# Kernel tuning notes

Measured on AMD Instinct MI355X. Metric: run time of the kernel, lower is better.

The kernel has to match this reference:

```python
import jax, jax.numpy as jnp
import numpy as np

B, D, OUT, K = 2048, 256, 256, 16


def setup_inputs() -> dict:
    key = jax.random.key(0)
    k1, k2, k3, k4 = jax.random.split(key, 4)
    x = jax.random.normal(k1, (B, D), dtype=jnp.float32)
    values = jax.random.uniform(k2, (OUT, D, K), dtype=jnp.float32, minval=-0.05, maxval=0.05)
    skip_w = jax.random.normal(k3, (OUT, D), dtype=jnp.float32) * (1.0 / np.sqrt(D).astype(np.float32))
    skip_b = jax.random.normal(k4, (OUT,), dtype=jnp.float32) * 0.01
    return {"x": x, "values": values, "skip_w": skip_w, "skip_b": skip_b}


def reference(x, values, skip_w, skip_b):
    # x: (B, D); values: (OUT, D, K); skip_w: (OUT, D); skip_b: (OUT,)
    num_knots = values.shape[-1]
    grid = jnp.linspace(-1.0, 1.0, num_knots)  # (K,)
    xc = jnp.clip(x, -1.0, 1.0)
    # torch.bucketize(x, grid) with right=False == searchsorted side='left'
    right = jnp.searchsorted(grid, xc, side='left')
    left = jnp.clip(right - 1, 0, num_knots - 2)  # (B, D)
    right = left + 1
    g0 = grid[left]
    g1 = grid[right]
    w = (xc - g0) / (g1 - g0 + 1e-12)  # (B, D)
    # Gather spline values per (sample, input-dim) knot bucket.
    vt = jnp.transpose(values, (1, 2, 0))  # (D, K, OUT)
    dim_idx = jnp.arange(xc.shape[1])[None, :]  # (1, D)
    v_left = vt[dim_idx, left]    # (B, D, OUT)
    v_right = vt[dim_idx, right]  # (B, D, OUT)
    # Linear interpolation + sum over input dims.
    y = jnp.sum((1.0 - w)[..., None] * v_left + w[..., None] * v_right, axis=1)  # (B, OUT)
    # Skip connection on the clamped input (torch reassigns x = clamp(x) first).
    return y + xc @ skip_w.T + skip_b
```

## Files before the change

### kernel.cpp

```cpp
#include <hip/hip_runtime.h>
#include <hip/hip_bf16.h>


namespace {
constexpr int Bsz  = 2048;
constexpr int Din  = 256;
constexpr int Dout = 256;
constexpr int Kn   = 16;
constexpr int KKNOT = Din * Kn;
constexpr int Ksp   = KKNOT + Din;
constexpr float INV_H = 7.5f;
constexpr float Hgrid = 2.0f / 15.0f;

constexpr int BM = 128, BN = 128, BK = 64;
constexpr int TOTSTEP = Ksp / BK;
constexpr int NSPLIT  = 17;
constexpr int MT = Bsz / BM;
constexpr int NT = Dout / BN;
}

typedef __attribute__((ext_vector_type(8))) short shortx8;
typedef __attribute__((ext_vector_type(4))) float floatx4;
typedef __attribute__((address_space(3))) unsigned int lds_u32;
typedef __attribute__((address_space(1))) const unsigned int gbl_u32;

__device__ __forceinline__ unsigned int f2bf(float f) {
  __hip_bfloat16 h = __float2bfloat16(f);
  return (unsigned int)*reinterpret_cast<unsigned short*>(&h);
}

__global__ __launch_bounds__(256) void build_wt(
    const float* __restrict__ values, const float* __restrict__ skip_w,
    unsigned short* __restrict__ Wt) {
  const int c = blockIdx.x * 256 + threadIdx.x;
  const float* src;
  unsigned short* dst;
  if (c < KKNOT * Dout / 8) {
    const int o = c >> 9, i = c & 511;
    src = values + (size_t)c * 8;
    dst = Wt + (size_t)o * Ksp + i * 8;
  } else {
    const int c2 = c - KKNOT * Dout / 8;
    const int o = c2 >> 5, i = c2 & 31;
    src = skip_w + (size_t)c2 * 8;
    dst = Wt + (size_t)o * Ksp + KKNOT + i * 8;
  }
  const float4 v0 = *(const float4*)src;
  const float4 v1 = *(const float4*)(src + 4);
  const unsigned int u0 = f2bf(v0.x) | (f2bf(v0.y) << 16);
  const unsigned int u1 = f2bf(v0.z) | (f2bf(v0.w) << 16);
  const unsigned int u2 = f2bf(v1.x) | (f2bf(v1.y) << 16);
  const unsigned int u3 = f2bf(v1.z) | (f2bf(v1.w) << 16);
  *(uint4*)dst = make_uint4(u0, u1, u2, u3);
}

__global__ __launch_bounds__(256) void kan_gemm(
    const float* __restrict__ x, const unsigned short* __restrict__ Wt,
    float* __restrict__ part) {
  __shared__ __align__(16) unsigned short As[BM][BK];
  __shared__ __align__(16) unsigned short Bs[BN][BK];

  const int tid = threadIdx.x;
  const int ks  = blockIdx.x % NSPLIT;
  const int nt  = (blockIdx.x / NSPLIT) % NT;
  const int mt  = blockIdx.x / (NSPLIT * NT);
  const int m0 = mt * BM, n0 = nt * BN;
  const int g0 = ks * (TOTSTEP / NSPLIT), g1 = g0 + TOTSTEP / NSPLIT;

  const int row  = tid & 127;
  const int half = tid >> 7;
  const int b    = m0 + row;

  const int wave = tid >> 6, lane = tid & 63;
  const int wm = (wave & 1) * 64, wn = (wave >> 1) * 64;
  const int lrow = lane & 15, lq = lane >> 4;

  floatx4 acc[4][4] = {};

  for (int g = g0; g < g1; ++g) {
    __syncthreads();

    #pragma unroll
    for (int p = 0; p < 4; ++p) {
      const int c = tid + p * 256;
      const int n = c >> 3, kcs = c & 7;
      const int kc = kcs ^ (n & 7);
      const unsigned short* gsrc = Wt + (size_t)(n0 + n) * Ksp + g * 64 + kc * 8;
      unsigned int* l = (unsigned int*)(&Bs[0][0]) + c * 4;
      __builtin_amdgcn_global_load_lds((gbl_u32*)gsrc, (lds_u32*)l, 16, 0, 0);
    }

    unsigned int u[16];
    if (g < KKNOT / BK) {
      const float2 tt = *(const float2*)(x + (size_t)b * Din + g * 4 + 2 * half);
      const float t0 = (fminf(1.f, fmaxf(-1.f, tt.x)) + 1.f) * INV_H;
      const float t1 = (fminf(1.f, fmaxf(-1.f, tt.y)) + 1.f) * INV_H;
      #pragma unroll
      for (int i = 0; i < 8; ++i) {
        const float a0 = fmaxf(0.f, 1.f - fabsf(t0 - (float)(2 * i)));
        const float a1 = fmaxf(0.f, 1.f - fabsf(t0 - (float)(2 * i + 1)));
        u[i] = f2bf(a0) | (f2bf(a1) << 16);
        const float b0 = fmaxf(0.f, 1.f - fabsf(t1 - (float)(2 * i)));
        const float b1 = fmaxf(0.f, 1.f - fabsf(t1 - (float)(2 * i + 1)));
        u[8 + i] = f2bf(b0) | (f2bf(b1) << 16);
      }
    } else {
      const int off = (g - KKNOT / BK) * 64 + half * 32;
      const float4* xq = (const float4*)(x + (size_t)b * Din + off);
      #pragma unroll
      for (int q = 0; q < 8; ++q) {
        const float4 v = xq[q];
        u[2 * q]     = f2bf(fminf(1.f, fmaxf(-1.f, v.x))) | (f2bf(fminf(1.f, fmaxf(-1.f, v.y))) << 16);
        u[2 * q + 1] = f2bf(fminf(1.f, fmaxf(-1.f, v.z))) | (f2bf(fminf(1.f, fmaxf(-1.f, v.w))) << 16);
      }
    }
    #pragma unroll
    for (int j = 0; j < 4; ++j) {
      const int slot = (half * 4 + j) ^ (row & 7);
      *(uint4*)((char*)(&As[0][0]) + row * 128 + slot * 16) =
          make_uint4(u[4 * j], u[4 * j + 1], u[4 * j + 2], u[4 * j + 3]);
    }

    __syncthreads();

    shortx8 af[4][2], bfr[4][2];
    #pragma unroll
    for (int i = 0; i < 4; ++i) {
      const int r = wm + 16 * i + lrow;
      #pragma unroll
      for (int kk = 0; kk < 2; ++kk) {
        const int slot = (kk * 4 + lq) ^ (r & 7);
        af[i][kk] = *(const shortx8*)((const char*)(&As[0][0]) + r * 128 + slot * 16);
      }
    }
    #pragma unroll
    for (int j = 0; j < 4; ++j) {
      const int r = wn + 16 * j + lrow;
      #pragma unroll
      for (int kk = 0; kk < 2; ++kk) {
        const int slot = (kk * 4 + lq) ^ (r & 7);
        bfr[j][kk] = *(const shortx8*)((const char*)(&Bs[0][0]) + r * 128 + slot * 16);
      }
    }
    #pragma unroll
    for (int kk = 0; kk < 2; ++kk)
      #pragma unroll
      for (int i = 0; i < 4; ++i)
        #pragma unroll
        for (int j = 0; j < 4; ++j)
          acc[i][j] = __builtin_amdgcn_mfma_f32_16x16x32_bf16(af[i][kk], bfr[j][kk], acc[i][j], 0, 0, 0);
  }

  float* P = part + (size_t)ks * Bsz * Dout;
  #pragma unroll
  for (int i = 0; i < 4; ++i) {
    const int grow = m0 + wm + 16 * i + lq * 4;
    #pragma unroll
    for (int j = 0; j < 4; ++j) {
      const int gcol = n0 + wn + 16 * j + lrow;
      #pragma unroll
      for (int r = 0; r < 4; ++r)
        P[(size_t)(grow + r) * Dout + gcol] = acc[i][j][r];
    }
  }
}

__global__ __launch_bounds__(256) void kan_reduce(
    const float* __restrict__ part, const float* __restrict__ skip_b,
    float* __restrict__ out) {
  const int i = blockIdx.x * 256 + threadIdx.x;
  const int base = i * 4;
  const int o = base & (Dout - 1);
  float4 a = *(const float4*)(skip_b + o);
  #pragma unroll
  for (int s = 0; s < NSPLIT; ++s) {
    const float4 p = *(const float4*)(part + (size_t)s * Bsz * Dout + base);
    a.x += p.x; a.y += p.y; a.z += p.z; a.w += p.w;
  }
  *(float4*)(out + base) = a;
}

__device__ __forceinline__ void knot_interp(float xraw, float& xv, float& w, int& l) {
  xv = fminf(1.0f, fmaxf(-1.0f, xraw));
  float t = (xv + 1.0f) * INV_H;
  l = (int)ceilf(t) - 1;
  l = l < 0 ? 0 : (l > Kn - 2 ? Kn - 2 : l);
  float g0 = -1.0f + Hgrid * (float)l;
  w = (xv - g0) * INV_H;
}

__global__ __launch_bounds__(256) void prep_transpose(
    const float* __restrict__ values, const float* __restrict__ skip_w,
    float* __restrict__ vt, float* __restrict__ swt) {
  int idx = blockIdx.x * blockDim.x + threadIdx.x;
  if (idx < Din * Kn * Dout) {
    int k = idx & (Kn - 1);
    int d = (idx >> 4) & (Din - 1);
    int o = idx >> 12;
    vt[(d * Kn + k) * Dout + o] = values[idx];
  }
  if (idx < Dout * Din) {
    int d = idx & (Din - 1);
    int o = idx >> 8;
    swt[d * Dout + o] = skip_w[idx];
  }
}

__global__ __launch_bounds__(256) void kan_main(
    const float* __restrict__ x, const float* __restrict__ vt,
    const float* __restrict__ swt, const float* __restrict__ skip_b,
    float* __restrict__ out) {
  __shared__ float s_w[4][Din];
  __shared__ float s_x[4][Din];
  __shared__ int   s_l[4][Din];
  const int tid = threadIdx.x;
  const int b0  = blockIdx.x * 4;
  for (int i = tid; i < 4 * Din; i += 256) {
    int bb = i >> 8;
    int d  = i & (Din - 1);
    float xv, w; int l;
    knot_interp(x[(b0 + bb) * Din + d], xv, w, l);
    s_w[bb][d] = w; s_x[bb][d] = xv; s_l[bb][d] = l;
  }
  __syncthreads();
  const int g = tid >> 6, lane = tid & 63;
  const int o = lane << 2, b = b0 + g;
  float4 acc = make_float4(0.f, 0.f, 0.f, 0.f);
  for (int d = 0; d < Din; ++d) {
    const float w = s_w[g][d], xv = s_x[g][d];
    const int l = s_l[g][d];
    const float* base = vt + (d * Kn + l) * Dout + o;
    const float4 vl = *(const float4*)(base);
    const float4 vr = *(const float4*)(base + Dout);
    const float4 sw = *(const float4*)(swt + d * Dout + o);
    acc.x = fmaf(xv, sw.x, fmaf(w, vr.x - vl.x, acc.x + vl.x));
    acc.y = fmaf(xv, sw.y, fmaf(w, vr.y - vl.y, acc.y + vl.y));
    acc.z = fmaf(xv, sw.z, fmaf(w, vr.z - vl.z, acc.z + vl.z));
    acc.w = fmaf(xv, sw.w, fmaf(w, vr.w - vl.w, acc.w + vl.w));
  }
  const float4 bias = *(const float4*)(skip_b + o);
  acc.x += bias.x; acc.y += bias.y; acc.z += bias.z; acc.w += bias.w;
  *(float4*)(out + (size_t)b * Dout + o) = acc;
}

extern "C" void kernel_launch(void* const* d_in, const int* in_sizes, int n_in,
                              void* d_out, int out_size, void* d_ws, size_t ws_size,
                              hipStream_t stream) {
  (void)in_sizes; (void)n_in; (void)out_size;
  const float* x      = (const float*)d_in[0];
  const float* values = (const float*)d_in[1];
  const float* skip_w = (const float*)d_in[2];
  const float* skip_b = (const float*)d_in[3];
  float* out = (float*)d_out;

  const size_t wt_bytes   = (size_t)Dout * Ksp * sizeof(unsigned short);
  const size_t part_bytes = (size_t)NSPLIT * Bsz * Dout * sizeof(float);
  const size_t need_gemm  = wt_bytes + part_bytes;
  const size_t need_fb    = (size_t)(Din * Kn * Dout + Din * Dout) * sizeof(float);

  if (ws_size >= need_gemm) {
    unsigned short* Wt = (unsigned short*)d_ws;
    float* part = (float*)((char*)d_ws + wt_bytes);
    build_wt<<<(KKNOT * Dout / 8 + Din * Dout / 8 + 255) / 256, 256, 0, stream>>>(values, skip_w, Wt);
    kan_gemm<<<MT * NT * NSPLIT, 256, 0, stream>>>(x, Wt, part);
    kan_reduce<<<Bsz * Dout / 4 / 256, 256, 0, stream>>>(part, skip_b, out);
  } else if (ws_size >= need_fb) {
    float* vt  = (float*)d_ws;
    float* swt = vt + Din * Kn * Dout;
    prep_transpose<<<(Din * Kn * Dout + 255) / 256, 256, 0, stream>>>(values, skip_w, vt, swt);
    kan_main<<<Bsz / 4, 256, 0, stream>>>(x, vt, swt, skip_b, out);
  }
}
```

Measured before the change: 85.14 us.

## Prepack weights into MFMA fragment layout and drop LDS from GEMM

The weight prep kernel now writes bf16 weights directly in the per-lane MFMA B-fragment order, so each wave loads its B operand straight from global memory into registers without staging in LDS. The hat-basis A fragments are generated per lane in registers. The GEMM moves to independent 64x64 per-wave tiles with register double-buffering and no __syncthreads. The split-K factor drops from 17 to 8, which shrinks the partial buffer the reduce kernel has to read. The trade-off is that the block-level operand reuse LDS provided is gone, so each wave does more global and L2 loads and recomputes its basis values.

Measured after the change: 102.2 us. +20.0%, slower.

```diff
diff --git a/kernel.cpp b/kernel.cpp
--- a/kernel.cpp
+++ b/kernel.cpp
@@ -9,155 +9,144 @@
 constexpr int Kn   = 16;
 constexpr int KKNOT = Din * Kn;
 constexpr int Ksp   = KKNOT + Din;
+constexpr int KB    = Ksp / 32;
 constexpr float INV_H = 7.5f;
 constexpr float Hgrid = 2.0f / 15.0f;
 
-constexpr int BM = 128, BN = 128, BK = 64;
-constexpr int TOTSTEP = Ksp / BK;
-constexpr int NSPLIT  = 17;
-constexpr int MT = Bsz / BM;
-constexpr int NT = Dout / BN;
+constexpr int NSPLIT = 8;
+constexpr int SPS    = KB / NSPLIT;
 }
 
 typedef __attribute__((ext_vector_type(8))) short shortx8;
 typedef __attribute__((ext_vector_type(4))) float floatx4;
-typedef __attribute__((address_space(3))) unsigned int lds_u32;
-typedef __attribute__((address_space(1))) const unsigned int gbl_u32;
 
 __device__ __forceinline__ unsigned int f2bf(float f) {
   __hip_bfloat16 h = __float2bfloat16(f);
   return (unsigned int)*reinterpret_cast<unsigned short*>(&h);
 }
-
-__global__ __launch_bounds__(256) void build_wt(
+__device__ __forceinline__ float clamp1(float v) {
+  return fminf(1.f, fmaxf(-1.f, v));
+}
+
+union FragCvt { uint4 u; shortx8 s; };
+
+__global__ __launch_bounds__(256) void kan_prep(
     const float* __restrict__ values, const float* __restrict__ skip_w,
-    unsigned short* __restrict__ Wt) {
-  const int c = blockIdx.x * 256 + threadIdx.x;
-  const float* src;
-  unsigned short* dst;
-  if (c < KKNOT * Dout / 8) {
-    const int o = c >> 9, i = c & 511;
-    src = values + (size_t)c * 8;
-    dst = Wt + (size_t)o * Ksp + i * 8;
-  } else {
-    const int c2 = c - KKNOT * Dout / 8;
-    const int o = c2 >> 5, i = c2 & 31;
-    src = skip_w + (size_t)c2 * 8;
-    dst = Wt + (size_t)o * Ksp + KKNOT + i * 8;
-  }
+    unsigned short* __restrict__ Wf) {
+  const int tid = blockIdx.x * 256 + threadIdx.x;
+  const int q  = tid & 3;
+  const int n  = (tid >> 2) & 15;
+  const int og = (tid >> 6) & 15;
+  const int kb = tid >> 10;
+  const int o  = og * 16 + n;
+  const int k0 = kb * 32 + q * 8;
+  const float* src = (kb < KKNOT / 32)
+      ? values + (size_t)o * KKNOT + k0
+      : skip_w + (size_t)o * Din + (k0 - KKNOT);
   const float4 v0 = *(const float4*)src;
   const float4 v1 = *(const float4*)(src + 4);
-  const unsigned int u0 = f2bf(v0.x) | (f2bf(v0.y) << 16);
-  const unsigned int u1 = f2bf(v0.z) | (f2bf(v0.w) << 16);
-  const unsigned int u2 = f2bf(v1.x) | (f2bf(v1.y) << 16);
-  const unsigned int u3 = f2bf(v1.z) | (f2bf(v1.w) << 16);
-  *(uint4*)dst = make_uint4(u0, u1, u2, u3);
+  const size_t chunk = (size_t)kb * 1024 + og * 64 + q * 16 + n;
+  *(uint4*)(Wf + chunk * 8) = make_uint4(
+      f2bf(v0.x) | (f2bf(v0.y) << 16), f2bf(v0.z) | (f2bf(v0.w) << 16),
+      f2bf(v1.x) | (f2bf(v1.y) << 16), f2bf(v1.z) | (f2bf(v1.w) << 16));
 }
 
 __global__ __launch_bounds__(256) void kan_gemm(
-    const float* __restrict__ x, const unsigned short* __restrict__ Wt,
+    const float* __restrict__ x, const unsigned short* __restrict__ Wf,
     float* __restrict__ part) {
-  __shared__ __align__(16) unsigned short As[BM][BK];
-  __shared__ __align__(16) unsigned short Bs[BN][BK];
-
-  const int tid = threadIdx.x;
-  const int ks  = blockIdx.x % NSPLIT;
-  const int nt  = (blockIdx.x / NSPLIT) % NT;
-  const int mt  = blockIdx.x / (NSPLIT * NT);
-  const int m0 = mt * BM, n0 = nt * BN;
-  const int g0 = ks * (TOTSTEP / NSPLIT), g1 = g0 + TOTSTEP / NSPLIT;
-
-  const int row  = tid & 127;
-  const int half = tid >> 7;
-  const int b    = m0 + row;
-
+  const int tid  = threadIdx.x;
   const int wave = tid >> 6, lane = tid & 63;
-  const int wm = (wave & 1) * 64, wn = (wave >> 1) * 64;
+  const int gw   = blockIdx.x * 4 + wave;
+  const int ks   = gw & 7;
+  const int ni   = (gw >> 3) & 3;
+  const int mi   = gw >> 5;
+  const int m0   = mi * 64;
+  const int og0  = ni * 4;
+  const int kb0  = ks * SPS, kb1 = kb0 + SPS;
+
   const int lrow = lane & 15, lq = lane >> 4;
+  const int dsel = lq >> 1;
+  const float hbase = (float)((lq & 1) * 8);
+
+  const uint4* B = (const uint4*)Wf;
 
   floatx4 acc[4][4] = {};
-
-  for (int g = g0; g < g1; ++g) {
-    __syncthreads();
-
+  uint4 bb[2][4];
+  float xs[2][4];
+
+  #pragma unroll
+  for (int j = 0; j < 4; ++j) bb[0][j] = B[(size_t)kb0 * 1024 + (og0 + j) * 64 + lane];
+  if (kb0 < KKNOT / 32) {
     #pragma unroll
-    for (int p = 0; p < 4; ++p) {
-      const int c = tid + p * 256;
-      const int n = c >> 3, kcs = c & 7;
-      const int kc = kcs ^ (n & 7);
-      const unsigned short* gsrc = Wt + (size_t)(n0 + n) * Ksp + g * 64 + kc * 8;
-      unsigned int* l = (unsigned int*)(&Bs[0][0]) + c * 4;
-      __builtin_amdgcn_global_load_lds((gbl_u32*)gsrc, (lds_u32*)l, 16, 0, 0);
-    }
-
-    unsigned int u[16];
-    if (g < KKNOT / BK) {
-      const float2 tt = *(const float2*)(x + (size_t)b * Din + g * 4 + 2 * half);
-      const float t0 = (fminf(1.f, fmaxf(-1.f, tt.x)) + 1.f) * INV_H;
-      const float t1 = (fminf(1.f, fmaxf(-1.f, tt.y)) + 1.f) * INV_H;
-      #pragma unroll
-      for (int i = 0; i < 8; ++i) {
-        const float a0 = fmaxf(0.f, 1.f - fabsf(t0 - (float)(2 * i)));
-        const float a1 = fmaxf(0.f, 1.f - fabsf(t0 - (float)(2 * i + 1)));
-        u[i] = f2bf(a0) | (f2bf(a1) << 16);
-        const float b0 = fmaxf(0.f, 1.f - fabsf(t1 - (float)(2 * i)));
-        const float b1 = fmaxf(0.f, 1.f - fabsf(t1 - (float)(2 * i + 1)));
-        u[8 + i] = f2bf(b0) | (f2bf(b1) << 16);
+    for (int i = 0; i < 4; ++i)
+      xs[0][i] = x[(size_t)(m0 + 16 * i + lrow) * Din + kb0 * 2 + dsel];
+  }
+
+  for (int s = 0; s < SPS; ++s) {
+    const int kb = kb0 + s;
+    const int cur = s & 1, nxt = cur ^ 1;
+
+    if (s + 1 < SPS) {
+      const int kn = kb + 1;
+      #pragma unroll
+      for (int j = 0; j < 4; ++j) bb[nxt][j] = B[(size_t)kn * 1024 + (og0 + j) * 64 + lane];
+      if (kn < KKNOT / 32) {
+        #pragma unroll
+        for (int i = 0; i < 4; ++i)
+          xs[nxt][i] = x[(size_t)(m0 + 16 * i + lrow) * Din + kn * 2 + dsel];
+      }
+    }
+
+    shortx8 af[4];
+    if (kb < KKNOT / 32) {
+      #pragma unroll
+      for (int i = 0; i < 4; ++i) {
+        const float t = (clamp1(xs[cur][i]) + 1.f) * INV_H;
+        FragCvt c;
+        unsigned int uu[4];
+        #pragma unroll
+        for (int p = 0; p < 4; ++p) {
+          const float e0 = fmaxf(0.f, 1.f - fabsf(t - (hbase + (float)(2 * p))));
+          const float e1 = fmaxf(0.f, 1.f - fabsf(t - (hbase + (float)(2 * p + 1))));
+          uu[p] = f2bf(e0) | (f2bf(e1) << 16);
+        }
+        c.u = make_uint4(uu[0], uu[1], uu[2], uu[3]);
+        af[i] = c.s;
       }
     } else {
-      const int off = (g - KKNOT / BK) * 64 + half * 32;
-      const float4* xq = (const float4*)(x + (size_t)b * Din + off);
-      #pragma unroll
-      for (int q = 0; q < 8; ++q) {
-        const float4 v = xq[q];
-        u[2 * q]     = f2bf(fminf(1.f, fmaxf(-1.f, v.x))) | (f2bf(fminf(1.f, fmaxf(-1.f, v.y))) << 16);
-        u[2 * q + 1] = f2bf(fminf(1.f, fmaxf(-1.f, v.z))) | (f2bf(fminf(1.f, fmaxf(-1.f, v.w))) << 16);
+      const int xoff = (kb - KKNOT / 32) * 32 + lq * 8;
+      #pragma unroll
+      for (int i = 0; i < 4; ++i) {
+        const float* xp = x + (size_t)(m0 + 16 * i + lrow) * Din + xoff;
+        const float4 v0 = *(const float4*)xp;
+        const float4 v1 = *(const float4*)(xp + 4);
+        FragCvt c;
+        c.u = make_uint4(
+            f2bf(clamp1(v0.x)) | (f2bf(clamp1(v0.y)) << 16),
+            f2bf(clamp1(v0.z)) | (f2bf(clamp1(v0.w)) << 16),
+            f2bf(clamp1(v1.x)) | (f2bf(clamp1(v1.y)) << 16),
+            f2bf(clamp1(v1.z)) | (f2bf(clamp1(v1.w)) << 16));
+        af[i] = c.s;
       }
     }
+
     #pragma unroll
     for (int j = 0; j < 4; ++j) {
-      const int slot = (half * 4 + j) ^ (row & 7);
-      *(uint4*)((char*)(&As[0][0]) + row * 128 + slot * 16) =
-          make_uint4(u[4 * j], u[4 * j + 1], u[4 * j + 2], u[4 * j + 3]);
-    }
-
-    __syncthreads();
-
-    shortx8 af[4][2], bfr[4][2];
-    #pragma unroll
-    for (int i = 0; i < 4; ++i) {
-      const int r = wm + 16 * i + lrow;
-      #pragma unroll
-      for (int kk = 0; kk < 2; ++kk) {
-        const int slot = (kk * 4 + lq) ^ (r & 7);
-        af[i][kk] = *(const shortx8*)((const char*)(&As[0][0]) + r * 128 + slot * 16);
-      }
-    }
-    #pragma unroll
-    for (int j = 0; j < 4; ++j) {
-      const int r = wn + 16 * j + lrow;
-      #pragma unroll
-      for (int kk = 0; kk < 2; ++kk) {
-        const int slot = (kk * 4 + lq) ^ (r & 7);
-        bfr[j][kk] = *(const shortx8*)((const char*)(&Bs[0][0]) + r * 128 + slot * 16);
-      }
-    }
-    #pragma unroll
-    for (int kk = 0; kk < 2; ++kk)
+      FragCvt bc; bc.u = bb[cur][j];
+      const shortx8 bf = bc.s;
       #pragma unroll
       for (int i = 0; i < 4; ++i)
-        #pragma unroll
-        for (int j = 0; j < 4; ++j)
-          acc[i][j] = __builtin_amdgcn_mfma_f32_16x16x32_bf16(af[i][kk], bfr[j][kk], acc[i][j], 0, 0, 0);
+        acc[i][j] = __builtin_amdgcn_mfma_f32_16x16x32_bf16(af[i], bf, acc[i][j], 0, 0, 0);
+    }
   }
 
   float* P = part + (size_t)ks * Bsz * Dout;
   #pragma unroll
   for (int i = 0; i < 4; ++i) {
-    const int grow = m0 + wm + 16 * i + lq * 4;
+    const int grow = m0 + 16 * i + lq * 4;
     #pragma unroll
     for (int j = 0; j < 4; ++j) {
-      const int gcol = n0 + wn + 16 * j + lrow;
+      const int gcol = og0 * 16 + 16 * j + lrow;
       #pragma unroll
       for (int r = 0; r < 4; ++r)
         P[(size_t)(grow + r) * Dout + gcol] = acc[i][j][r];
@@ -253,16 +242,16 @@
   const float* skip_b = (const float*)d_in[3];
   float* out = (float*)d_out;
 
-  const size_t wt_bytes   = (size_t)Dout * Ksp * sizeof(unsigned short);
+  const size_t wf_bytes   = (size_t)Dout * Ksp * sizeof(unsigned short);
   const size_t part_bytes = (size_t)NSPLIT * Bsz * Dout * sizeof(float);
-  const size_t need_gemm  = wt_bytes + part_bytes;
+  const size_t need_gemm  = wf_bytes + part_bytes;
   const size_t need_fb    = (size_t)(Din * Kn * Dout + Din * Dout) * sizeof(float);
 
   if (ws_size >= need_gemm) {
-    unsigned short* Wt = (unsigned short*)d_ws;
-    float* part = (float*)((char*)d_ws + wt_bytes);
-    build_wt<<<(KKNOT * Dout / 8 + Din * Dout / 8 + 255) / 256, 256, 0, stream>>>(values, skip_w, Wt);
-    kan_gemm<<<MT * NT * NSPLIT, 256, 0, stream>>>(x, Wt, part);
+    unsigned short* Wf = (unsigned short*)d_ws;
+    float* part = (float*)((char*)d_ws + wf_bytes);
+    kan_prep<<<(KB * 1024) / 256, 256, 0, stream>>>(values, skip_w, Wf);
+    kan_gemm<<<256, 256, 0, stream>>>(x, Wf, part);
     kan_reduce<<<Bsz * Dout / 4 / 256, 256, 0, stream>>>(part, skip_b, out);
   } else if (ws_size >= need_fb) {
     float* vt  = (float*)d_ws;
```
